# Kernel tuning notes

Hardware: AMD Instinct MI355X
Metric: run time of the kernel (lower is better)

The kernel has to match this reference:

```python
import jax, jax.numpy as jnp
import numpy as np

B, C, D, H, W = 4, 320, 16, 16, 16
E, DK, DV = 2, 32, 160  # heads, key dim, value dim
EPS = 1e-6


def setup_inputs() -> dict:
    key = jax.random.key(0)
    ks = jax.random.split(key, 8)
    s_in = 1.0 / np.sqrt(C)
    s_mg = 1.0 / np.sqrt(E * DV)
    return {
        "x": jax.random.normal(ks[0], (B, C, D, H, W), jnp.float32),
        # pointwise (1x1x1) conv weights, stacked over heads
        "Wq": jax.random.normal(ks[1], (E, DK, C), jnp.float32) * s_in,
        "bq": jax.random.normal(ks[2], (E, DK), jnp.float32) * 0.01,
        "Wk": jax.random.normal(ks[3], (E, DK, C), jnp.float32) * s_in,
        "bk": jax.random.normal(ks[4], (E, DK), jnp.float32) * 0.01,
        "Wv": jax.random.normal(ks[5], (E, DV, C), jnp.float32) * s_in,
        "bv": jax.random.normal(ks[6], (E, DV), jnp.float32) * 0.01,
        # merging 1x1x1 conv: dv*num_heads -> C
        "Wm": jax.random.normal(ks[7], (C, E * DV), jnp.float32) * s_mg,
        "bm": jnp.zeros((C,), jnp.float32),
    }


def reference(x, Wq, bq, Wk, bk, Wv, bv, Wm, bm):
    b, c = x.shape[0], x.shape[1]
    xf = x.reshape(b, c, -1)  # [B, C, N], N = prod(spatial)

    def proj(Wt, bt):
        # 1x1x1 conv over all heads at once: [B, E, d, N]
        return jnp.einsum('ekc,bcn->bekn', Wt, xf) + bt[None, :, :, None]

    Q = proj(Wq, bq)
    K = proj(Wk, bk)
    V = proj(Wv, bv)  # [B, E, DV, N]

    def l2norm(t):
        # F.normalize over channel dim (dim=1 of [B, dk, N] per head)
        n = jnp.linalg.norm(t, axis=2, keepdims=True)
        return t / jnp.maximum(n, EPS)

    Qn = l2norm(Q)
    Kn = l2norm(K)

    # spatial attention: contract over key channels -> [B, E, N, N]
    A = jax.nn.softmax(jnp.einsum('bekn,bekm->benm', Qn, Kn), axis=-1)
    R = jnp.einsum('benm,bevm->bevn', A, V)  # [B, E, DV, N]

    # concat heads along channel dim, then merge conv + residual
    Rcat = R.reshape(b, E * DV, -1)  # [B, E*DV, N]
    out = jnp.einsum('cf,bfn->bcn', Wm, Rcat) + bm[None, :, None]
    return out.reshape(x.shape) + x
```

## Files before the change

kernel.cpp:

```cpp
#include <hip/hip_runtime.h>
#include <hip/hip_bf16.h>

#define BN 4
#define CN 320
#define NN 4096
#define EN 2
#define DKN 32
#define DVN 160

typedef __bf16 bf16;
typedef __bf16 bf16x8 __attribute__((ext_vector_type(8)));
typedef __bf16 bf16x4 __attribute__((ext_vector_type(4)));
typedef float f32x4 __attribute__((ext_vector_type(4)));

static __device__ __forceinline__ f32x4 mfma16(bf16x8 a, bf16x8 b, f32x4 c) {
  return __builtin_amdgcn_mfma_f32_16x16x32_bf16(a, b, c, 0, 0, 0);
}


__global__ __launch_bounds__(256) void k_prep(
    const float* __restrict__ Wq, const float* __restrict__ bq,
    const float* __restrict__ Wk, const float* __restrict__ bk,
    const float* __restrict__ Wv, const float* __restrict__ bv,
    const float* __restrict__ Wm,
    bf16* __restrict__ W_all, bf16* __restrict__ Wm_bf, float* __restrict__ b_all) {
  int t = blockIdx.x * 256 + threadIdx.x;
  if (t < 448 * CN) {
    int r = t / CN;
    float v;
    if (r < 64) v = Wq[t];
    else if (r < 128) v = Wk[t - 64 * CN];
    else v = Wv[t - 128 * CN];
    W_all[t] = (bf16)v;
  }
  if (t < 320 * 320) Wm_bf[t] = (bf16)Wm[t];
  if (t < 448) {
    float v;
    if (t < 64) v = bq[t];
    else if (t < 128) v = bk[t - 64];
    else v = bv[t - 128];
    b_all[t] = v;
  }
}

__global__ __launch_bounds__(256) void k_xt(const float* __restrict__ x, bf16* __restrict__ xT) {
  int blk = blockIdx.x;
  int b = blk / 640;
  int rem = blk - b * 640;
  int cc = rem >> 4;
  int nb = rem & 15;
  int n = nb * 256 + threadIdx.x;
  const float* xp = x + ((size_t)b * CN + cc * 8) * NN + n;
  bf16x8 v;
#pragma unroll
  for (int j = 0; j < 8; j++) v[j] = (bf16)xp[(size_t)j * NN];
  *(bf16x8*)(xT + ((size_t)b * NN + n) * CN + cc * 8) = v;
}

__global__ __launch_bounds__(256) void k_proj(
    const bf16* __restrict__ W_all, const float* __restrict__ b_all,
    const bf16* __restrict__ xT, float* __restrict__ QK, bf16* __restrict__ Vc) {
  int blk = blockIdx.x;
  int b = blk / 448;
  int rem = blk - b * 448;
  int mt = rem >> 4, nb = rem & 15;
  int w = threadIdx.x >> 6, l = threadIdx.x & 63;
  int lg = l >> 4, lr = l & 15;
  int m0 = mt * 16;
  int n0 = nb * 256 + w * 64;
  f32x4 acc[4] = {};
  const bf16* wp = W_all + (m0 + lr) * CN + 8 * lg;
  const bf16* xp = xT + ((size_t)b * NN + n0 + lr) * CN + 8 * lg;
#pragma unroll 2
  for (int c0 = 0; c0 < CN; c0 += 32) {
    bf16x8 a = *(const bf16x8*)(wp + c0);
#pragma unroll
    for (int j = 0; j < 4; j++) {
      bf16x8 bb = *(const bf16x8*)(xp + j * 16 * CN + c0);
      acc[j] = mfma16(a, bb, acc[j]);
    }
  }
#pragma unroll
  for (int i = 0; i < 4; i++) {
    int row = m0 + 4 * lg + i;
    float bias = b_all[row];
    if (row < 128) {
      float* qk = QK + ((size_t)b * 128 + row) * NN + n0 + lr;
#pragma unroll
      for (int j = 0; j < 4; j++) qk[j * 16] = acc[j][i] + bias;
    } else {
      int rr = row - 128;
      int e = rr / 160, dvl = rr - e * 160;
      int vt = dvl >> 4, lrc = dvl & 15;
      size_t beI = (size_t)(b * 2 + e);
#pragma unroll
      for (int j = 0; j < 4; j++) {
        int key = n0 + j * 16 + lr;
        int T = key >> 5, h = (key >> 4) & 1, g = (key >> 2) & 3, ic = key & 3;
        Vc[(((beI * 128 + T) * 10 + vt) * 4 + g) * 128 + lrc * 8 + h * 4 + ic] =
            (bf16)(acc[j][i] + bias);
      }
    }
  }
}

__global__ __launch_bounds__(256) void k_norm(
    const float* __restrict__ QK, bf16* __restrict__ Qn, bf16* __restrict__ Kn) {
  int t = blockIdx.x * 256 + threadIdx.x;
  int isk = t >> 15;
  int r = t & 32767;
  int b = r >> 13, e = (r >> 12) & 1, n = r & (NN - 1);
  const float* p = QK + ((size_t)b * 128 + isk * 64 + e * 32) * NN + n;
  float v[32];
  float ss = 0.f;
#pragma unroll
  for (int d = 0; d < 32; d++) { float q = p[(size_t)d * NN]; v[d] = q; ss += q * q; }
  float s = 1.0f / fmaxf(sqrtf(ss), 1e-6f);
  bf16* o = (isk ? Kn : Qn) + ((size_t)(b * 2 + e) * NN + n) * 32;
#pragma unroll
  for (int d0 = 0; d0 < 32; d0 += 8) {
    bf16x8 vo;
#pragma unroll
    for (int j = 0; j < 8; j++) vo[j] = (bf16)(v[d0 + j] * s);
    *(bf16x8*)(o + d0) = vo;
  }
}

__global__ __launch_bounds__(256) void k_attn(
    const bf16* __restrict__ Qn, const bf16* __restrict__ Kn,
    const bf16* __restrict__ Vc, bf16* __restrict__ Rt) {
  __shared__ float sbuf[64][83];
  int blk = blockIdx.x;
  int be = blk >> 7, qc = blk & 127;
  int w = threadIdx.x >> 6, l = threadIdx.x & 63;
  int lg = l >> 4, lr = l & 15;
  int qb = qc * 32;
  const bf16* qbase = Qn + ((size_t)be * NN + qb) * 32 + 8 * lg;
  bf16x8 qf0 = *(const bf16x8*)(qbase + lr * 32);
  bf16x8 qf1 = *(const bf16x8*)(qbase + (16 + lr) * 32);
  const bf16* kbase = Kn + (size_t)be * NN * 32 + 8 * lg;
  const bf16* vbase = Vc + (size_t)be * (128 * 10 * 512) + (size_t)l * 8;
  int mstart = w * (NN / 4), mend = mstart + (NN / 4);
  f32x4 acc0[10] = {};
  f32x4 acc1[10] = {};
  float rs0 = 0.f, rs1 = 0.f;
  bf16x8 kf0 = *(const bf16x8*)(kbase + (size_t)(mstart + lr) * 32);
  bf16x8 kf1 = *(const bf16x8*)(kbase + (size_t)(mstart + 16 + lr) * 32);
  for (int m0 = mstart; m0 < mend; m0 += 32) {
    const bf16* vp = vbase + (size_t)(m0 >> 5) * (10 * 512);
    bf16x8 vf[10];
#pragma unroll
    for (int vt = 0; vt < 10; vt++) vf[vt] = *(const bf16x8*)(vp + vt * 512);
    f32x4 zero = {};
    f32x4 s00 = mfma16(kf0, qf0, zero);
    f32x4 s01 = mfma16(kf1, qf0, zero);
    f32x4 s10 = mfma16(kf0, qf1, zero);
    f32x4 s11 = mfma16(kf1, qf1, zero);
    if (m0 + 32 < mend) {
      kf0 = *(const bf16x8*)(kbase + (size_t)(m0 + 32 + lr) * 32);
      kf1 = *(const bf16x8*)(kbase + (size_t)(m0 + 48 + lr) * 32);
    }
    bf16x8 pf0, pf1;
#pragma unroll
    for (int i = 0; i < 4; i++) {
      float e00 = __expf(s00[i]), e01 = __expf(s01[i]);
      float e10 = __expf(s10[i]), e11 = __expf(s11[i]);
      rs0 += e00 + e01;
      rs1 += e10 + e11;
      pf0[i] = (bf16)e00; pf0[4 + i] = (bf16)e01;
      pf1[i] = (bf16)e10; pf1[4 + i] = (bf16)e11;
    }
#pragma unroll
    for (int vt = 0; vt < 10; vt++) {
      acc0[vt] = mfma16(pf0, vf[vt], acc0[vt]);
      acc1[vt] = mfma16(pf1, vf[vt], acc1[vt]);
    }
  }
  for (int r = 1; r < 4; ++r) {
    if (w == r) {
      float* p = &sbuf[l][0];
#pragma unroll
      for (int vt = 0; vt < 10; vt++)
#pragma unroll
        for (int i = 0; i < 4; i++) {
          p[vt * 4 + i] = acc0[vt][i];
          p[40 + vt * 4 + i] = acc1[vt][i];
        }
      p[80] = rs0; p[81] = rs1;
    }
    __syncthreads();
    if (w == 0) {
      const float* p = &sbuf[l][0];
#pragma unroll
      for (int vt = 0; vt < 10; vt++)
#pragma unroll
        for (int i = 0; i < 4; i++) {
          acc0[vt][i] += p[vt * 4 + i];
          acc1[vt][i] += p[40 + vt * 4 + i];
        }
      rs0 += p[80]; rs1 += p[81];
    }
    __syncthreads();
  }
  if (w == 0) {
    rs0 += __shfl_xor(rs0, 16); rs0 += __shfl_xor(rs0, 32);
    rs1 += __shfl_xor(rs1, 16); rs1 += __shfl_xor(rs1, 32);
    f32x4 rinv0, rinv1;
#pragma unroll
    for (int i = 0; i < 4; i++) {
      rinv0[i] = 1.0f / __shfl(rs0, 4 * lg + i);
      rinv1[i] = 1.0f / __shfl(rs1, 4 * lg + i);
    }
    int b = be >> 1, e = be & 1;
#pragma unroll
    for (int vt = 0; vt < 10; vt++) {
#pragma unroll
      for (int i = 0; i < 4; i++) {
        int q0 = qb + 4 * lg + i;
        int q1 = qb + 16 + 4 * lg + i;
        Rt[((size_t)b * NN + q0) * 320 + e * 160 + vt * 16 + lr] = (bf16)(acc0[vt][i] * rinv0[i]);
        Rt[((size_t)b * NN + q1) * 320 + e * 160 + vt * 16 + lr] = (bf16)(acc1[vt][i] * rinv1[i]);
      }
    }
  }
}

__global__ __launch_bounds__(256) void k_merge(
    const bf16* __restrict__ Wm_bf, const float* __restrict__ bm,
    const bf16* __restrict__ Rt, const float* __restrict__ x, float* __restrict__ out) {
  int blk = blockIdx.x;
  int b = blk / 320;
  int rem = blk - b * 320;
  int ct = rem >> 4, nb = rem & 15;
  int w = threadIdx.x >> 6, l = threadIdx.x & 63;
  int lg = l >> 4, lr = l & 15;
  int c0 = ct * 16, n0 = nb * 256 + w * 64;
  f32x4 acc[4] = {};
  const bf16* ap = Wm_bf + (c0 + lr) * 320 + 8 * lg;
  const bf16* bp = Rt + ((size_t)b * NN + n0 + lr) * 320 + 8 * lg;
#pragma unroll 2
  for (int f0 = 0; f0 < 320; f0 += 32) {
    bf16x8 a = *(const bf16x8*)(ap + f0);
#pragma unroll
    for (int j = 0; j < 4; j++) {
      bf16x8 bb = *(const bf16x8*)(bp + j * 16 * 320 + f0);
      acc[j] = mfma16(a, bb, acc[j]);
    }
  }
#pragma unroll
  for (int i = 0; i < 4; i++) {
    int c = c0 + 4 * lg + i;
    float bias = bm[c];
    const float* xp = x + ((size_t)b * 320 + c) * NN + n0 + lr;
    float* op = out + ((size_t)b * 320 + c) * NN + n0 + lr;
#pragma unroll
    for (int j = 0; j < 4; j++) op[j * 16] = acc[j][i] + bias + xp[j * 16];
  }
}

extern "C" void kernel_launch(void* const* d_in, const int* in_sizes, int n_in,
                              void* d_out, int out_size, void* d_ws, size_t ws_size,
                              hipStream_t stream) {
  const float* x  = (const float*)d_in[0];
  const float* Wq = (const float*)d_in[1];
  const float* bq = (const float*)d_in[2];
  const float* Wk = (const float*)d_in[3];
  const float* bk = (const float*)d_in[4];
  const float* Wv = (const float*)d_in[5];
  const float* bv = (const float*)d_in[6];
  const float* Wm = (const float*)d_in[7];
  const float* bm = (const float*)d_in[8];
  float* out = (float*)d_out;
  char* ws = (char*)d_ws;
  bf16*  W_all = (bf16*)(ws + 0);
  bf16*  Wm_bf = (bf16*)(ws + 286720);
  float* b_all = (float*)(ws + 491520);
  bf16*  xT    = (bf16*)(ws + 493568);
  float* QK    = (float*)(ws + 10979328);
  bf16*  Qn    = (bf16*)(ws + 19367936);
  bf16*  Kn    = (bf16*)(ws + 21465088);
  bf16*  Vc    = (bf16*)(ws + 23562240);
  bf16*  Rt    = (bf16*)(ws + 34048000);

  k_prep<<<560, 256, 0, stream>>>(Wq, bq, Wk, bk, Wv, bv, Wm, W_all, Wm_bf, b_all);
  k_xt<<<2560, 256, 0, stream>>>(x, xT);
  k_proj<<<1792, 256, 0, stream>>>(W_all, b_all, xT, QK, Vc);
  k_norm<<<256, 256, 0, stream>>>(QK, Qn, Kn);
  k_attn<<<1024, 256, 0, stream>>>(Qn, Kn, Vc, Rt);
  k_merge<<<1280, 256, 0, stream>>>(Wm_bf, bm, Rt, x, out);
}
```

Baseline: 235.1 us.

## Share K/V tiles across waves via double-buffered LDS staging in attention

Measured after the change: 249.9 us. +6.3%, slower.

```diff
diff --git a/kernel.cpp b/kernel.cpp
--- a/kernel.cpp
+++ b/kernel.cpp
@@ -10,7 +10,6 @@
 
 typedef __bf16 bf16;
 typedef __bf16 bf16x8 __attribute__((ext_vector_type(8)));
-typedef __bf16 bf16x4 __attribute__((ext_vector_type(4)));
 typedef float f32x4 __attribute__((ext_vector_type(4)));
 
 static __device__ __forceinline__ f32x4 mfma16(bf16x8 a, bf16x8 b, f32x4 c) {
@@ -105,7 +104,7 @@
 }
 
 __global__ __launch_bounds__(256) void k_norm(
-    const float* __restrict__ QK, bf16* __restrict__ Qn, bf16* __restrict__ Kn) {
+    const float* __restrict__ QK, bf16* __restrict__ Qn, bf16* __restrict__ Kc) {
   int t = blockIdx.x * 256 + threadIdx.x;
   int isk = t >> 15;
   int r = t & 32767;
@@ -116,113 +115,103 @@
 #pragma unroll
   for (int d = 0; d < 32; d++) { float q = p[(size_t)d * NN]; v[d] = q; ss += q * q; }
   float s = 1.0f / fmaxf(sqrtf(ss), 1e-6f);
-  bf16* o = (isk ? Kn : Qn) + ((size_t)(b * 2 + e) * NN + n) * 32;
-#pragma unroll
-  for (int d0 = 0; d0 < 32; d0 += 8) {
-    bf16x8 vo;
-#pragma unroll
-    for (int j = 0; j < 8; j++) vo[j] = (bf16)(v[d0 + j] * s);
-    *(bf16x8*)(o + d0) = vo;
+  if (!isk) {
+    bf16* o = Qn + ((size_t)(b * 2 + e) * NN + n) * 32;
+#pragma unroll
+    for (int d0 = 0; d0 < 32; d0 += 8) {
+      bf16x8 vo;
+#pragma unroll
+      for (int j = 0; j < 8; j++) vo[j] = (bf16)(v[d0 + j] * s);
+      *(bf16x8*)(o + d0) = vo;
+    }
+  } else {
+    bf16* kc = Kc + ((size_t)(b * 2 + e) * 128 + (n >> 5)) * 1024 + ((n >> 4) & 1) * 512 +
+               (n & 15) * 8;
+#pragma unroll
+    for (int o = 0; o < 4; o++) {
+      bf16x8 vo;
+#pragma unroll
+      for (int j = 0; j < 8; j++) vo[j] = (bf16)(v[o * 8 + j] * s);
+      *(bf16x8*)(kc + o * 128) = vo;
+    }
   }
 }
 
 __global__ __launch_bounds__(256) void k_attn(
-    const bf16* __restrict__ Qn, const bf16* __restrict__ Kn,
+    const bf16* __restrict__ Qn, const bf16* __restrict__ Kc,
     const bf16* __restrict__ Vc, bf16* __restrict__ Rt) {
-  __shared__ float sbuf[64][83];
-  int blk = blockIdx.x;
-  int be = blk >> 7, qc = blk & 127;
+  __shared__ __align__(16) char smem[2][12288];
+  int blk = blockIdx.x;
+  int be = blk >> 6, qblk = blk & 63;
   int w = threadIdx.x >> 6, l = threadIdx.x & 63;
   int lg = l >> 4, lr = l & 15;
-  int qb = qc * 32;
-  const bf16* qbase = Qn + ((size_t)be * NN + qb) * 32 + 8 * lg;
-  bf16x8 qf0 = *(const bf16x8*)(qbase + lr * 32);
-  bf16x8 qf1 = *(const bf16x8*)(qbase + (16 + lr) * 32);
-  const bf16* kbase = Kn + (size_t)be * NN * 32 + 8 * lg;
-  const bf16* vbase = Vc + (size_t)be * (128 * 10 * 512) + (size_t)l * 8;
-  int mstart = w * (NN / 4), mend = mstart + (NN / 4);
-  f32x4 acc0[10] = {};
-  f32x4 acc1[10] = {};
-  float rs0 = 0.f, rs1 = 0.f;
-  bf16x8 kf0 = *(const bf16x8*)(kbase + (size_t)(mstart + lr) * 32);
-  bf16x8 kf1 = *(const bf16x8*)(kbase + (size_t)(mstart + 16 + lr) * 32);
-  for (int m0 = mstart; m0 < mend; m0 += 32) {
-    const bf16* vp = vbase + (size_t)(m0 >> 5) * (10 * 512);
-    bf16x8 vf[10];
-#pragma unroll
-    for (int vt = 0; vt < 10; vt++) vf[vt] = *(const bf16x8*)(vp + vt * 512);
+  int qb = qblk * 64 + w * 16;
+  bf16x8 qf = *(const bf16x8*)(Qn + ((size_t)be * NN + qb + lr) * 32 + 8 * lg);
+  const char* kbase = (const char*)Kc + (size_t)be * 128 * 2048;
+  const char* vbase = (const char*)Vc + (size_t)be * 128 * 10240;
+  int ch = w * 3;
+  f32x4 acc[10] = {};
+  float rs = 0.f;
+#pragma unroll
+  for (int c = 0; c < 3; c++) {
+    int chunk = ch + c;
+    const char* src = (chunk < 2) ? (kbase + chunk * 1024 + l * 16)
+                                  : (vbase + (chunk - 2) * 1024 + l * 16);
+    __builtin_amdgcn_global_load_lds(
+        (const __attribute__((address_space(1))) void*)src,
+        (__attribute__((address_space(3))) void*)(&smem[0][chunk * 1024 + l * 16]), 16, 0, 0);
+  }
+  __syncthreads();
+  for (int T = 0; T < 128; T++) {
+    int cur = T & 1;
+    if (T + 1 < 128) {
+      const char* kt = kbase + (size_t)(T + 1) * 2048;
+      const char* vt_ = vbase + (size_t)(T + 1) * 10240;
+#pragma unroll
+      for (int c = 0; c < 3; c++) {
+        int chunk = ch + c;
+        const char* src = (chunk < 2) ? (kt + chunk * 1024 + l * 16)
+                                      : (vt_ + (chunk - 2) * 1024 + l * 16);
+        __builtin_amdgcn_global_load_lds(
+            (const __attribute__((address_space(1))) void*)src,
+            (__attribute__((address_space(3))) void*)(&smem[cur ^ 1][chunk * 1024 + l * 16]),
+            16, 0, 0);
+      }
+    }
+    const bf16* Kl = (const bf16*)(&smem[cur][0]);
+    const bf16* Vl = (const bf16*)(&smem[cur][2048]);
+    bf16x8 kf0 = *(const bf16x8*)(Kl + l * 8);
+    bf16x8 kf1 = *(const bf16x8*)(Kl + 512 + l * 8);
     f32x4 zero = {};
-    f32x4 s00 = mfma16(kf0, qf0, zero);
-    f32x4 s01 = mfma16(kf1, qf0, zero);
-    f32x4 s10 = mfma16(kf0, qf1, zero);
-    f32x4 s11 = mfma16(kf1, qf1, zero);
-    if (m0 + 32 < mend) {
-      kf0 = *(const bf16x8*)(kbase + (size_t)(m0 + 32 + lr) * 32);
-      kf1 = *(const bf16x8*)(kbase + (size_t)(m0 + 48 + lr) * 32);
-    }
-    bf16x8 pf0, pf1;
+    f32x4 s0 = mfma16(kf0, qf, zero);
+    f32x4 s1 = mfma16(kf1, qf, zero);
+    bf16x8 pf;
 #pragma unroll
     for (int i = 0; i < 4; i++) {
-      float e00 = __expf(s00[i]), e01 = __expf(s01[i]);
-      float e10 = __expf(s10[i]), e11 = __expf(s11[i]);
-      rs0 += e00 + e01;
-      rs1 += e10 + e11;
-      pf0[i] = (bf16)e00; pf0[4 + i] = (bf16)e01;
-      pf1[i] = (bf16)e10; pf1[4 + i] = (bf16)e11;
+      float e0 = __expf(s0[i]), e1 = __expf(s1[i]);
+      rs += e0 + e1;
+      pf[i] = (bf16)e0; pf[4 + i] = (bf16)e1;
     }
 #pragma unroll
     for (int vt = 0; vt < 10; vt++) {
-      acc0[vt] = mfma16(pf0, vf[vt], acc0[vt]);
-      acc1[vt] = mfma16(pf1, vf[vt], acc1[vt]);
-    }
-  }
-  for (int r = 1; r < 4; ++r) {
-    if (w == r) {
-      float* p = &sbuf[l][0];
-#pragma unroll
-      for (int vt = 0; vt < 10; vt++)
-#pragma unroll
-        for (int i = 0; i < 4; i++) {
-          p[vt * 4 + i] = acc0[vt][i];
-          p[40 + vt * 4 + i] = acc1[vt][i];
-        }
-      p[80] = rs0; p[81] = rs1;
+      bf16x8 vf = *(const bf16x8*)(Vl + vt * 512 + l * 8);
+      acc[vt] = mfma16(pf, vf, acc[vt]);
     }
     __syncthreads();
-    if (w == 0) {
-      const float* p = &sbuf[l][0];
-#pragma unroll
-      for (int vt = 0; vt < 10; vt++)
-#pragma unroll
-        for (int i = 0; i < 4; i++) {
-          acc0[vt][i] += p[vt * 4 + i];
-          acc1[vt][i] += p[40 + vt * 4 + i];
-        }
-      rs0 += p[80]; rs1 += p[81];
-    }
-    __syncthreads();
-  }
-  if (w == 0) {
-    rs0 += __shfl_xor(rs0, 16); rs0 += __shfl_xor(rs0, 32);
-    rs1 += __shfl_xor(rs1, 16); rs1 += __shfl_xor(rs1, 32);
-    f32x4 rinv0, rinv1;
+  }
+  rs += __shfl_xor(rs, 16);
+  rs += __shfl_xor(rs, 32);
+  f32x4 rinv;
+#pragma unroll
+  for (int i = 0; i < 4; i++) rinv[i] = 1.0f / __shfl(rs, 4 * lg + i);
+  int b = be >> 1, e = be & 1;
+#pragma unroll
+  for (int vt = 0; vt < 10; vt++)
 #pragma unroll
     for (int i = 0; i < 4; i++) {
-      rinv0[i] = 1.0f / __shfl(rs0, 4 * lg + i);
-      rinv1[i] = 1.0f / __shfl(rs1, 4 * lg + i);
-    }
-    int b = be >> 1, e = be & 1;
-#pragma unroll
-    for (int vt = 0; vt < 10; vt++) {
-#pragma unroll
-      for (int i = 0; i < 4; i++) {
-        int q0 = qb + 4 * lg + i;
-        int q1 = qb + 16 + 4 * lg + i;
-        Rt[((size_t)b * NN + q0) * 320 + e * 160 + vt * 16 + lr] = (bf16)(acc0[vt][i] * rinv0[i]);
-        Rt[((size_t)b * NN + q1) * 320 + e * 160 + vt * 16 + lr] = (bf16)(acc1[vt][i] * rinv1[i]);
-      }
-    }
-  }
+      int q = qb + 4 * lg + i;
+      Rt[((size_t)b * NN + q) * 320 + e * 160 + vt * 16 + lr] = (bf16)(acc[vt][i] * rinv[i]);
+    }
 }
 
 __global__ __launch_bounds__(256) void k_merge(
@@ -278,14 +267,14 @@
   bf16*  xT    = (bf16*)(ws + 493568);
   float* QK    = (float*)(ws + 10979328);
   bf16*  Qn    = (bf16*)(ws + 19367936);
-  bf16*  Kn    = (bf16*)(ws + 21465088);
+  bf16*  Kc    = (bf16*)(ws + 21465088);
   bf16*  Vc    = (bf16*)(ws + 23562240);
   bf16*  Rt    = (bf16*)(ws + 34048000);
 
   k_prep<<<560, 256, 0, stream>>>(Wq, bq, Wk, bk, Wv, bv, Wm, W_all, Wm_bf, b_all);
   k_xt<<<2560, 256, 0, stream>>>(x, xT);
   k_proj<<<1792, 256, 0, stream>>>(W_all, b_all, xT, QK, Vc);
-  k_norm<<<256, 256, 0, stream>>>(QK, Qn, Kn);
-  k_attn<<<1024, 256, 0, stream>>>(Qn, Kn, Vc, Rt);
+  k_norm<<<256, 256, 0, stream>>>(QK, Qn, Kc);
+  k_attn<<<512, 256, 0, stream>>>(Qn, Kc, Vc, Rt);
   k_merge<<<1280, 256, 0, stream>>>(Wm_bf, bm, Rt, x, out);
 }
```
